# Optimization experiments

Hardware: AMD Instinct MI355X
Metric: run time of the kernel (lower is better)

## Reference

```python
import jax, jax.numpy as jnp
import numpy as np

C = 1024
H = 16
D = C // H  # head_dim = 64
FF = 4 * C


def setup_inputs() -> dict:
    key = jax.random.key(0)
    ks = jax.random.split(key, 10)
    s = lambda fan_in: 1.0 / np.sqrt(fan_in)
    return {
        "x": jax.random.normal(ks[0], (2, 2048, C), dtype=jnp.float32),
        "ln1_g": jnp.ones((C,), jnp.float32),
        "ln1_b": jnp.zeros((C,), jnp.float32),
        "w_qkv": jax.random.normal(ks[1], (C, 3 * C), jnp.float32) * s(C),
        "w_proj": jax.random.normal(ks[2], (C, C), jnp.float32) * s(C),
        "b_proj": jnp.zeros((C,), jnp.float32),
        "ln2_g": jnp.ones((C,), jnp.float32),
        "ln2_b": jnp.zeros((C,), jnp.float32),
        "w_fc1": jax.random.normal(ks[3], (C, FF), jnp.float32) * s(C),
        "b_fc1": jnp.zeros((FF,), jnp.float32),
        "w_fc2": jax.random.normal(ks[4], (FF, C), jnp.float32) * s(FF),
        "b_fc2": jnp.zeros((C,), jnp.float32),
    }


def _layernorm(x, g, b, eps=1e-5):
    mu = jnp.mean(x, axis=-1, keepdims=True)
    var = jnp.var(x, axis=-1, keepdims=True)
    return (x - mu) * jax.lax.rsqrt(var + eps) * g + b


def reference(x, ln1_g, ln1_b, w_qkv, w_proj, b_proj, ln2_g, ln2_b, w_fc1, b_fc1, w_fc2, b_fc2):
    B, N, _ = x.shape
    scale = D ** -0.5
    # --- attention sub-block (pre-LN) ---
    h = _layernorm(x, ln1_g, ln1_b)
    qkv = (h @ w_qkv).reshape(B, N, 3, H, D)
    q, k, v = jnp.moveaxis(qkv, 2, 0)          # each [B, N, H, D]
    attn = jnp.einsum("bnhd,bmhd->bhnm", q, k) * scale  # [B,H,N,N]
    attn = jax.nn.softmax(attn, axis=-1)
    o = jnp.einsum("bhnm,bmhd->bnhd", attn, v).reshape(B, N, C)
    x = x + o @ w_proj + b_proj
    # --- MLP sub-block (pre-LN) ---
    h = _layernorm(x, ln2_g, ln2_b)
    h = jax.nn.gelu(h @ w_fc1 + b_fc1, approximate=False)
    x = x + h @ w_fc2 + b_fc2
    return x
```

## Files before the change

kernel.cpp:

```cpp
#include <hip/hip_runtime.h>
#include <hip/hip_bf16.h>

typedef unsigned short u16;
typedef unsigned int u32;
typedef __attribute__((ext_vector_type(8))) short bf16x8;
typedef __attribute__((ext_vector_type(4))) float f32x4;
typedef __attribute__((ext_vector_type(4))) int   i32x4;
typedef __attribute__((ext_vector_type(4))) float fvec4;
typedef __attribute__((ext_vector_type(4))) unsigned int u32x4;

__device__ inline u16 f2bf(float f) {
    union { float f; unsigned u; } v; v.f = f;
    unsigned r = v.u + 0x7fffu + ((v.u >> 16) & 1u);
    return (u16)(r >> 16);
}

__device__ inline u32 cvtpk(float lo, float hi) {
    u32 r;
    asm("v_cvt_pk_bf16_f32 %0, %1, %2" : "=v"(r) : "v"(lo), "v"(hi));
    return r;
}

__device__ inline f32x4 mfma16(bf16x8 a, bf16x8 b, f32x4 c) {
    return __builtin_amdgcn_mfma_f32_16x16x32_bf16(a, b, c, 0, 0, 0);
}

__device__ inline void gload16(const void* g, void* l) {
    __builtin_amdgcn_global_load_lds(
        (const __attribute__((address_space(1))) unsigned int*)g,
        (__attribute__((address_space(3))) unsigned int*)l, 16, 0, 0);
}

__global__ __launch_bounds__(256)
void transpose_all(const float* __restrict__ w0, u16* __restrict__ o0,
                   const float* __restrict__ w1, u16* __restrict__ o1,
                   const float* __restrict__ w2, u16* __restrict__ o2,
                   const float* __restrict__ w3, u16* __restrict__ o3) {
    __shared__ float tile[32][33];
    int b = blockIdx.x;
    const float* in; u16* out; int K, N, local;
    if (b < 3072)      { in = w0; out = o0; K = 1024; N = 3072; local = b; }
    else if (b < 4096) { in = w1; out = o1; K = 1024; N = 1024; local = b - 3072; }
    else if (b < 8192) { in = w2; out = o2; K = 1024; N = 4096; local = b - 4096; }
    else               { in = w3; out = o3; K = 4096; N = 1024; local = b - 8192; }
    const int nx = N >> 5;
    const int n0 = (local % nx) * 32, k0 = (local / nx) * 32;
    const int x = threadIdx.x & 31, y = threadIdx.x >> 5;
    for (int i = 0; i < 4; ++i)
        tile[y + i * 8][x] = in[(size_t)(k0 + y + i * 8) * N + n0 + x];
    __syncthreads();
    for (int i = 0; i < 4; ++i) {
        int r = y + i * 8;
        out[(size_t)(n0 + r) * K + k0 + x] = f2bf(tile[x][r]);
    }
}

__global__ __launch_bounds__(256)
void vtrans(const u16* __restrict__ qkv, u16* __restrict__ vT) {
    __shared__ u32 tl[64][33];
    const int t0 = blockIdx.x * 64, f0 = blockIdx.y * 64;
    const int a = threadIdx.x & 31, yy = threadIdx.x >> 5;
    for (int i = 0; i < 8; ++i) {
        int t = yy + i * 8;
        tl[t][a] = *(const u32*)(qkv + (size_t)(t0 + t) * 3072 + 2048 + f0 + a * 2);
    }
    __syncthreads();
    for (int i = 0; i < 8; ++i) {
        int f = yy + i * 8;
        u32 lo = tl[2 * a][f >> 1], hi = tl[2 * a + 1][f >> 1];
        u32 r = (f & 1) ? ((lo >> 16) | (hi & 0xffff0000u))
                        : ((lo & 0xffffu) | (hi << 16));
        *(u32*)(vT + (size_t)(f0 + f) * 4096 + t0 + 2 * a) = r;
    }
}

__global__ __launch_bounds__(256)
void ln_kernel(const float* __restrict__ x, const float* __restrict__ g,
               const float* __restrict__ bvec, u16* __restrict__ out) {
    __shared__ float red[2][4];
    const int row = blockIdx.x, tid = threadIdx.x;
    const float* xr = x + (size_t)row * 1024;
    fvec4 v = *(const fvec4*)(xr + tid * 4);
    float s  = v[0] + v[1] + v[2] + v[3];
    float s2 = v[0]*v[0] + v[1]*v[1] + v[2]*v[2] + v[3]*v[3];
    for (int off = 1; off < 64; off <<= 1) {
        s  += __shfl_xor(s,  off);
        s2 += __shfl_xor(s2, off);
    }
    const int w = tid >> 6;
    if ((tid & 63) == 0) { red[0][w] = s; red[1][w] = s2; }
    __syncthreads();
    s  = red[0][0] + red[0][1] + red[0][2] + red[0][3];
    s2 = red[1][0] + red[1][1] + red[1][2] + red[1][3];
    const float mu  = s * (1.0f / 1024.0f);
    const float var = s2 * (1.0f / 1024.0f) - mu * mu;
    const float rstd = rsqrtf(var + 1e-5f);
    fvec4 gv = *(const fvec4*)(g + tid * 4);
    fvec4 bv = *(const fvec4*)(bvec + tid * 4);
    u16 o4[4];
    for (int i = 0; i < 4; ++i)
        o4[i] = f2bf((v[i] - mu) * rstd * gv[i] + bv[i]);
    u32 lo = (u32)o4[0] | ((u32)o4[1] << 16);
    u32 hi = (u32)o4[2] | ((u32)o4[3] << 16);
    u32* dst = (u32*)(out + (size_t)row * 1024 + tid * 4);
    dst[0] = lo; dst[1] = hi;
}

__global__ __launch_bounds__(256)
void reduce4(const float* __restrict__ p1, const float* __restrict__ p2,
             const float* __restrict__ p3, const float* __restrict__ bias,
             const float* __restrict__ res, float* __restrict__ out) {
    const size_t base = (size_t)blockIdx.x * 1024 + threadIdx.x * 4;
    fvec4 a = *(const fvec4*)(out + base);
    fvec4 b = *(const fvec4*)(p1 + base);
    fvec4 c = *(const fvec4*)(p2 + base);
    fvec4 d = *(const fvec4*)(p3 + base);
    fvec4 r = *(const fvec4*)(res + base);
    fvec4 bi = *(const fvec4*)(bias + threadIdx.x * 4);
    fvec4 o;
#pragma unroll
    for (int i = 0; i < 4; ++i) o[i] = ((a[i] + b[i]) + (c[i] + d[i])) + bi[i] + r[i];
    *(fvec4*)(out + base) = o;
}

template <int MODE, int WM, int WN, int MT, int NT, int NYP>
__global__ __launch_bounds__(256)
void gemm64(const u16* __restrict__ A, const u16* __restrict__ Bt,
            const float* __restrict__ bias, const float* __restrict__ res,
            void* __restrict__ out, int M, int N, int K) {
    constexpr int TM = WM * MT * 16;
    constexpr int TN = WN * NT * 16;
    constexpr int AJ = TM / 64;
    constexpr int BJ = TN / 64;
    static_assert(TM == 128, "swizzle assumes 32 M-tiles");
    __shared__ __attribute__((aligned(16))) u16 sA[2 * TM * 32];
    __shared__ __attribute__((aligned(16))) u16 sB[2 * TN * 32];
    const int id = blockIdx.x;
    const int j  = id >> 3;
    const int by = (id & 7) * NYP + (j >> 5);
    const int bx = j & 31;
    const int tid = threadIdx.x;
    const int lane = tid & 63, w = tid >> 6;
    const int wm = w / WN, wn = w % WN;
    const int q = lane >> 4, l16 = lane & 15;

    f32x4 acc[MT][NT];
#pragma unroll
    for (int i = 0; i < MT; ++i)
#pragma unroll
        for (int jj = 0; jj < NT; ++jj) acc[i][jj] = (f32x4)0.0f;

    const int sr = lane >> 2;
    const int kc = (lane & 3) * 8;
    const u16* gA[AJ];
    const u16* gB[BJ];
#pragma unroll
    for (int jj = 0; jj < AJ; ++jj)
        gA[jj] = A + (size_t)(bx * TM + (jj * 4 + w) * 16 + sr) * K + kc;
#pragma unroll
    for (int jj = 0; jj < BJ; ++jj)
        gB[jj] = Bt + (size_t)(by * TN + (jj * 4 + w) * 16 + sr) * K + kc;

    for (int k0 = 0; k0 < K; k0 += 64) {
#pragma unroll
        for (int kt = 0; kt < 2; ++kt) {
#pragma unroll
            for (int jj = 0; jj < AJ; ++jj)
                gload16(gA[jj] + k0 + kt * 32, &sA[kt * TM * 32 + (jj * 4 + w) * 512]);
#pragma unroll
            for (int jj = 0; jj < BJ; ++jj)
                gload16(gB[jj] + k0 + kt * 32, &sB[kt * TN * 32 + (jj * 4 + w) * 512]);
        }
        __syncthreads();
#pragma unroll
        for (int kt = 0; kt < 2; ++kt) {
            bf16x8 af[MT], bf[NT];
#pragma unroll
            for (int mt = 0; mt < MT; ++mt)
                af[mt] = *(const bf16x8*)&sA[kt * TM * 32 +
                         (wm * MT * 16 + mt * 16 + l16) * 32 + q * 8];
#pragma unroll
            for (int nt = 0; nt < NT; ++nt)
                bf[nt] = *(const bf16x8*)&sB[kt * TN * 32 +
                         (wn * NT * 16 + nt * 16 + l16) * 32 + q * 8];
#pragma unroll
            for (int mt = 0; mt < MT; ++mt)
#pragma unroll
                for (int nt = 0; nt < NT; ++nt)
                    acc[mt][nt] = mfma16(af[mt], bf[nt], acc[mt][nt]);
        }
        __syncthreads();
    }

#pragma unroll
    for (int mt = 0; mt < MT; ++mt)
#pragma unroll
        for (int nt = 0; nt < NT; ++nt)
#pragma unroll
            for (int r = 0; r < 4; ++r) {
                const int row = bx * TM + wm * MT * 16 + mt * 16 + q * 4 + r;
                const int col = by * TN + wn * NT * 16 + nt * 16 + l16;
                const size_t idx = (size_t)row * N + col;
                float v = acc[mt][nt][r];
                if (MODE == 0) {
                    ((u16*)out)[idx] = f2bf(v);
                } else if (MODE == 1) {
                    ((float*)out)[idx] = v + bias[col] + res[idx];
                } else {
                    float t = v + bias[col];
                    ((u16*)out)[idx] = f2bf(t * 0.5f * (1.0f + erff(t * 0.70710678118f)));
                }
            }
}

template <int MODE, int SPLIT>
__global__ __launch_bounds__(512)
void gemm256(const u16* __restrict__ A, const u16* __restrict__ Bt,
             const float* __restrict__ bias, const float* __restrict__ res,
             void* __restrict__ out,
             float* __restrict__ q1, float* __restrict__ q2, float* __restrict__ q3,
             int M, int N, int K, int Kc) {
    __shared__ __attribute__((aligned(16))) u16 sA[2][16384];
    __shared__ __attribute__((aligned(16))) u16 sB[2][16384];
    const int tid  = threadIdx.x;
    const int w    = tid >> 6, lane = tid & 63;
    const int wm   = w >> 2,  wn   = w & 3;
    const int q    = lane >> 4, l16 = lane & 15;
    const int w8   = w << 3,  l8   = lane >> 3;
    const int kch  = (lane & 7) ^ l8;

    const int nwg  = gridDim.x;
    const int id   = blockIdx.x;
    const int wgid = (id & 7) * (nwg >> 3) + (id >> 3);
    int bx, by, sp;
    if (SPLIT == 1) { bx = wgid & 15; by = wgid >> 4; sp = 0; }
    else            { bx = wgid & 15; by = (wgid >> 4) & 3; sp = wgid >> 6; }

    const u16* pAs = A  + (size_t)(bx * 256 + w8 + l8) * K + kch * 8 + (size_t)sp * Kc;
    const u16* pBs = Bt + (size_t)(by * 256 + w8 + l8) * K + kch * 8 + (size_t)sp * Kc;

    const int cs0  = ((q ^ (l16 & 7)) << 4);
    const int cs1  = cs0 ^ 64;
    const int aoff = (wm * 128 + l16) * 128;
    const int boff = (wn * 64  + l16) * 128;

    f32x4 acc[8][4];
#pragma unroll
    for (int m = 0; m < 8; ++m)
#pragma unroll
        for (int n = 0; n < 4; ++n) acc[m][n] = (f32x4)0.0f;

#define GISS(P, r0, k0, SH, b_) \
    gload16((P) + (size_t)((r0) * K + (k0)), &SH[b_][((r0) + w8) * 64])

    GISS(pBs, 0, 0, sB, 0);  GISS(pBs, 64, 0, sB, 0);
    GISS(pBs, 128, 0, sB, 0); GISS(pBs, 192, 0, sB, 0);
    GISS(pAs, 0, 0, sA, 0);  GISS(pAs, 64, 0, sA, 0);
    GISS(pAs, 128, 0, sA, 0); GISS(pAs, 192, 0, sA, 0);
    GISS(pBs, 0, 64, sB, 1); GISS(pBs, 64, 64, sB, 1);
    GISS(pBs, 128, 64, sB, 1); GISS(pBs, 192, 64, sB, 1);
    asm volatile("s_waitcnt vmcnt(4)" ::: "memory");
    __builtin_amdgcn_s_barrier();

    bf16x8 bfr[4][2];

#define PHASE(mq_, cb_, SP, SH, sb_, sr0, sk0) do {                          \
    const char* bA_ = (const char*)&sA[cb_][0] + aoff;                       \
    const char* bB_ = (const char*)&sB[cb_][0] + boff;                       \
    if ((mq_) == 0) {                                                        \
        _Pragma("unroll") for (int n = 0; n < 4; ++n) {                      \
            bfr[n][0] = *(const bf16x8*)(bB_ + n * 2048 + cs0);              \
            bfr[n][1] = *(const bf16x8*)(bB_ + n * 2048 + cs1);              \
        }                                                                    \
    }                                                                        \
    bf16x8 af_[2][2];                                                        \
    _Pragma("unroll") for (int mi = 0; mi < 2; ++mi) {                       \
        af_[mi][0] = *(const bf16x8*)(bA_ + (2 * (mq_) + mi) * 2048 + cs0);  \
        af_[mi][1] = *(const bf16x8*)(bA_ + (2 * (mq_) + mi) * 2048 + cs1);  \
    }                                                                        \
    GISS(SP, (sr0), (sk0), SH, sb_);                                         \
    GISS(SP, (sr0) + 64, (sk0), SH, sb_);                                    \
    __builtin_amdgcn_sched_barrier(0);   \
    __builtin_amdgcn_s_barrier();                                            \
    asm volatile("s_waitcnt lgkmcnt(0)" ::: "memory");                       \
    __builtin_amdgcn_sched_barrier(0);          \
    __builtin_amdgcn_s_setprio(1);                                           \
    _Pragma("unroll") for (int kt = 0; kt < 2; ++kt)                         \
        _Pragma("unroll") for (int mi = 0; mi < 2; ++mi)                     \
            _Pragma("unroll") for (int n = 0; n < 4; ++n)                    \
                acc[2 * (mq_) + mi][n] =                                     \
                    mfma16(af_[mi][kt], bfr[n][kt], acc[2 * (mq_) + mi][n]); \
    __builtin_amdgcn_s_setprio(0);                                           \
    if ((mq_) == 3) asm volatile("s_waitcnt vmcnt(4)" ::: "memory");         \
    __builtin_amdgcn_s_barrier();                                            \
} while (0)

    const int NI = Kc >> 7;
    for (int i = 0; i < NI; ++i) {
        const int kb  = i << 7;
        const int kA1 = kb + 64;
        const int kN  = (kb + 128 < Kc) ? kb + 128 : Kc - 64;
        const int kB1 = (kb + 192 < Kc) ? kb + 192 : Kc - 64;
        PHASE(0, 0, pAs, sA, 1, 0,   kA1);
        PHASE(1, 0, pAs, sA, 1, 128, kA1);
        PHASE(2, 0, pBs, sB, 0, 0,   kN);
        PHASE(3, 0, pBs, sB, 0, 128, kN);
        PHASE(0, 1, pAs, sA, 0, 0,   kN);
        PHASE(1, 1, pAs, sA, 0, 128, kN);
        PHASE(2, 1, pBs, sB, 1, 0,   kB1);
        PHASE(3, 1, pBs, sB, 1, 128, kB1);
    }
#undef PHASE
#undef GISS

    float* po = nullptr;
    if (MODE == 3)
        po = sp == 0 ? (float*)out : sp == 1 ? q1 : sp == 2 ? q2 : q3;

#pragma unroll
    for (int m = 0; m < 8; ++m)
#pragma unroll
        for (int n = 0; n < 4; ++n)
#pragma unroll
            for (int r = 0; r < 4; ++r) {
                const int row = bx * 256 + wm * 128 + m * 16 + q * 4 + r;
                const int col = by * 256 + wn * 64 + n * 16 + l16;
                const size_t idx = (size_t)row * N + col;
                float v = acc[m][n][r];
                if (MODE == 0) {
                    ((u16*)out)[idx] = f2bf(v);
                } else if (MODE == 1) {
                    ((float*)out)[idx] = v + bias[col] + res[idx];
                } else if (MODE == 2) {
                    float t = v + bias[col];
                    ((u16*)out)[idx] = f2bf(t * 0.5f * (1.0f + erff(t * 0.70710678118f)));
                } else {
                    po[idx] = v;
                }
            }
}

__global__ __launch_bounds__(256)
void attention3(const u16* __restrict__ qkv, const u16* __restrict__ vT,
                u16* __restrict__ o) {
    __shared__ __attribute__((aligned(16))) u16 sK[64][72];
    __shared__ __attribute__((aligned(16))) u16 sV[64][72];

    const int tid = threadIdx.x;
    const int lane = tid & 63, w = tid >> 6;
    const int qc = lane >> 4, l16 = lane & 15;
    const int bx = blockIdx.x;
    const int qt = bx & 15, h = (bx >> 4) & 15, b = bx >> 8;
    const int rowbase = qt * 128 + w * 32;

    bf16x8 aQ[2][2];
#pragma unroll
    for (int mtq = 0; mtq < 2; ++mtq)
#pragma unroll
        for (int kd = 0; kd < 2; ++kd)
            aQ[mtq][kd] = *(const bf16x8*)(qkv +
                (size_t)(b * 2048 + rowbase + mtq * 16 + l16) * 3072 +
                h * 64 + kd * 32 + qc * 8);

    f32x4 accO[2][4];
#pragma unroll
    for (int mtq = 0; mtq < 2; ++mtq)
#pragma unroll
        for (int dt = 0; dt < 4; ++dt) accO[mtq][dt] = (f32x4)0.0f;
    f32x4 accS[2];
    accS[0] = (f32x4)0.0f; accS[1] = (f32x4)0.0f;

    bf16x8 vone;
#pragma unroll
    for (int i = 0; i < 8; ++i) vone[i] = (short)0x3F80;

    const int srr = tid >> 3;
    const int sc8 = (tid & 7) * 8;
    const u16* gK = qkv + (size_t)(b * 2048 + srr) * 3072 + 1024 + h * 64 + sc8;
    const u16* gV = vT + (size_t)(h * 64 + srr) * 4096 + b * 2048 + sc8;

    i32x4 cK[2], cV[2];
    cK[0] = *(const i32x4*)gK;
    cK[1] = *(const i32x4*)(gK + (size_t)32 * 3072);
    cV[0] = *(const i32x4*)gV;
    cV[1] = *(const i32x4*)(gV + (size_t)32 * 4096);

    const int sig_base = ((l16 >> 2) << 3) + (l16 & 3);

    for (int kc = 0; kc < 32; ++kc) {
        __syncthreads();
        *(i32x4*)&sK[srr][sc8]      = cK[0];
        *(i32x4*)&sK[srr + 32][sc8] = cK[1];
        *(i32x4*)&sV[srr][sc8]      = cV[0];
        *(i32x4*)&sV[srr + 32][sc8] = cV[1];
        const int kn = (kc + 1 < 32) ? kc + 1 : 31;
        i32x4 nK[2], nV[2];
        nK[0] = *(const i32x4*)(gK + (size_t)kn * 64 * 3072);
        nK[1] = *(const i32x4*)(gK + ((size_t)kn * 64 + 32) * 3072);
        nV[0] = *(const i32x4*)(gV + kn * 64);
        nV[1] = *(const i32x4*)(gV + (size_t)32 * 4096 + kn * 64);
        __syncthreads();

        bf16x8 kf[4][2];
#pragma unroll
        for (int mk = 0; mk < 4; ++mk) {
            const int krow = ((mk & 1) << 5) + ((mk >> 1) << 2) + sig_base;
            kf[mk][0] = *(const bf16x8*)&sK[krow][qc * 8];
            kf[mk][1] = *(const bf16x8*)&sK[krow][32 + qc * 8];
        }

        f32x4 s[2][4];
#pragma unroll
        for (int mtq = 0; mtq < 2; ++mtq)
#pragma unroll
            for (int mk = 0; mk < 4; ++mk) {
                f32x4 z = (f32x4)0.0f;
                z = mfma16(kf[mk][0], aQ[mtq][0], z);
                z = mfma16(kf[mk][1], aQ[mtq][1], z);
                s[mtq][mk] = z;
            }

        bf16x8 pf[2][2];
#pragma unroll
        for (int mtq = 0; mtq < 2; ++mtq) {
#pragma unroll
            for (int mk = 0; mk < 4; ++mk)
#pragma unroll
                for (int r = 0; r < 4; ++r)
                    s[mtq][mk][r] = __expf(s[mtq][mk][r] * 0.125f);
#pragma unroll
            for (int kt = 0; kt < 2; ++kt) {
                u32x4 pw;
                pw[0] = cvtpk(s[mtq][kt][0],     s[mtq][kt][1]);
                pw[1] = cvtpk(s[mtq][kt][2],     s[mtq][kt][3]);
                pw[2] = cvtpk(s[mtq][2 + kt][0], s[mtq][2 + kt][1]);
                pw[3] = cvtpk(s[mtq][2 + kt][2], s[mtq][2 + kt][3]);
                pf[mtq][kt] = *(const bf16x8*)&pw;
            }
        }

#pragma unroll
        for (int kt = 0; kt < 2; ++kt) {
#pragma unroll
            for (int dt = 0; dt < 4; ++dt) {
                bf16x8 vf = *(const bf16x8*)&sV[dt * 16 + l16][kt * 32 + qc * 8];
#pragma unroll
                for (int mtq = 0; mtq < 2; ++mtq)
                    accO[mtq][dt] = mfma16(pf[mtq][kt], vf, accO[mtq][dt]);
            }
#pragma unroll
            for (int mtq = 0; mtq < 2; ++mtq)
                accS[mtq] = mfma16(pf[mtq][kt], vone, accS[mtq]);
        }

        cK[0] = nK[0]; cK[1] = nK[1];
        cV[0] = nV[0]; cV[1] = nV[1];
    }

#pragma unroll
    for (int mtq = 0; mtq < 2; ++mtq)
#pragma unroll
        for (int r = 0; r < 4; ++r) {
            const float inv = 1.0f / accS[mtq][r];
            const size_t tok = (size_t)b * 2048 + rowbase + mtq * 16 + qc * 4 + r;
#pragma unroll
            for (int dt = 0; dt < 4; ++dt)
                o[tok * 1024 + h * 64 + dt * 16 + l16] = f2bf(accO[mtq][dt][r] * inv);
        }
}

extern "C" void kernel_launch(void* const* d_in, const int* in_sizes, int n_in,
                              void* d_out, int out_size, void* d_ws, size_t ws_size,
                              hipStream_t stream) {
    const float* x      = (const float*)d_in[0];
    const float* ln1_g  = (const float*)d_in[1];
    const float* ln1_b  = (const float*)d_in[2];
    const float* w_qkv  = (const float*)d_in[3];
    const float* w_proj = (const float*)d_in[4];
    const float* b_proj = (const float*)d_in[5];
    const float* ln2_g  = (const float*)d_in[6];
    const float* ln2_b  = (const float*)d_in[7];
    const float* w_fc1  = (const float*)d_in[8];
    const float* b_fc1  = (const float*)d_in[9];
    const float* w_fc2  = (const float*)d_in[10];
    const float* b_fc2  = (const float*)d_in[11];
    float* out = (float*)d_out;

    char* ws = (char*)d_ws;
    u16*   wqkvT  = (u16*)(ws + 0);
    u16*   wprojT = (u16*)(ws + 6291456);
    u16*   wfc1T  = (u16*)(ws + 8388608);
    u16*   wfc2T  = (u16*)(ws + 16777216);
    u16*   hA     = (u16*)(ws + 25165824);
    u16*   qkv    = (u16*)(ws + 33554432);
    float* x1     = (float*)(ws + 58720256);
    u16*   gbuf   = (u16*)(ws + 75497472);
    u16*   vT     = (u16*)(ws + 75497472);
    float* p1     = (float*)(ws + 0);
    float* p2     = (float*)(ws + 25165824);
    float* p3     = (float*)(ws + 41943040);

    dim3 blk(256);
    transpose_all<<<12288, blk, 0, stream>>>(w_qkv, wqkvT, w_proj, wprojT,
                                             w_fc1, wfc1T, w_fc2, wfc2T);

    ln_kernel<<<4096, blk, 0, stream>>>(x, ln1_g, ln1_b, hA);
    gemm256<0, 1><<<192, dim3(512), 0, stream>>>(hA, wqkvT, nullptr, nullptr, qkv,
                                                 nullptr, nullptr, nullptr, 4096, 3072, 1024, 1024);
    vtrans<<<dim3(64, 16), blk, 0, stream>>>(qkv, vT);
    attention3<<<512, blk, 0, stream>>>(qkv, vT, hA);
    gemm64<1, 4, 1, 2, 4, 2><<<512, blk, 0, stream>>>(hA, wprojT, b_proj, x, x1, 4096, 1024, 1024);

    u16* h2 = qkv;
    ln_kernel<<<4096, blk, 0, stream>>>(x1, ln2_g, ln2_b, h2);
    gemm256<2, 1><<<256, dim3(512), 0, stream>>>(h2, wfc1T, b_fc1, nullptr, gbuf,
                                                 nullptr, nullptr, nullptr, 4096, 4096, 1024, 1024);
    gemm256<3, 4><<<256, dim3(512), 0, stream>>>(gbuf, wfc2T, nullptr, nullptr, out,
                                                 p1, p2, p3, 4096, 1024, 4096, 1024);
    reduce4<<<4096, blk, 0, stream>>>(p1, p2, p3, b_fc2, x1, out);
}
```

Measured before the change: 357.0 us.

## Restructure GEMM main loop into two half-tile phases per K step

```diff
diff --git a/kernel.cpp b/kernel.cpp
--- a/kernel.cpp
+++ b/kernel.cpp
@@ -253,64 +253,72 @@
 #define GISS(P, r0, k0, SH, b_) \
     gload16((P) + (size_t)((r0) * K + (k0)), &SH[b_][((r0) + w8) * 64])
 
-    GISS(pBs, 0, 0, sB, 0);  GISS(pBs, 64, 0, sB, 0);
+    GISS(pBs, 0, 0, sB, 0);   GISS(pBs, 64, 0, sB, 0);
     GISS(pBs, 128, 0, sB, 0); GISS(pBs, 192, 0, sB, 0);
-    GISS(pAs, 0, 0, sA, 0);  GISS(pAs, 64, 0, sA, 0);
+    GISS(pAs, 0, 0, sA, 0);   GISS(pAs, 64, 0, sA, 0);
     GISS(pAs, 128, 0, sA, 0); GISS(pAs, 192, 0, sA, 0);
-    GISS(pBs, 0, 64, sB, 1); GISS(pBs, 64, 64, sB, 1);
-    GISS(pBs, 128, 64, sB, 1); GISS(pBs, 192, 64, sB, 1);
+    GISS(pBs, 0, 64, sB, 1);  GISS(pBs, 64, 64, sB, 1);
+    GISS(pBs, 128, 64, sB, 1);GISS(pBs, 192, 64, sB, 1);
     asm volatile("s_waitcnt vmcnt(4)" ::: "memory");
     __builtin_amdgcn_s_barrier();
 
-    bf16x8 bfr[4][2];
-
-#define PHASE(mq_, cb_, SP, SH, sb_, sr0, sk0) do {                          \
-    const char* bA_ = (const char*)&sA[cb_][0] + aoff;                       \
-    const char* bB_ = (const char*)&sB[cb_][0] + boff;                       \
-    if ((mq_) == 0) {                                                        \
-        _Pragma("unroll") for (int n = 0; n < 4; ++n) {                      \
-            bfr[n][0] = *(const bf16x8*)(bB_ + n * 2048 + cs0);              \
-            bfr[n][1] = *(const bf16x8*)(bB_ + n * 2048 + cs1);              \
-        }                                                                    \
-    }                                                                        \
-    bf16x8 af_[2][2];                                                        \
-    _Pragma("unroll") for (int mi = 0; mi < 2; ++mi) {                       \
-        af_[mi][0] = *(const bf16x8*)(bA_ + (2 * (mq_) + mi) * 2048 + cs0);  \
-        af_[mi][1] = *(const bf16x8*)(bA_ + (2 * (mq_) + mi) * 2048 + cs1);  \
-    }                                                                        \
-    GISS(SP, (sr0), (sk0), SH, sb_);                                         \
-    GISS(SP, (sr0) + 64, (sk0), SH, sb_);                                    \
-    __builtin_amdgcn_sched_barrier(0);   \
-    __builtin_amdgcn_s_barrier();                                            \
-    asm volatile("s_waitcnt lgkmcnt(0)" ::: "memory");                       \
-    __builtin_amdgcn_sched_barrier(0);          \
-    __builtin_amdgcn_s_setprio(1);                                           \
-    _Pragma("unroll") for (int kt = 0; kt < 2; ++kt)                         \
-        _Pragma("unroll") for (int mi = 0; mi < 2; ++mi)                     \
-            _Pragma("unroll") for (int n = 0; n < 4; ++n)                    \
-                acc[2 * (mq_) + mi][n] =                                     \
-                    mfma16(af_[mi][kt], bfr[n][kt], acc[2 * (mq_) + mi][n]); \
-    __builtin_amdgcn_s_setprio(0);                                           \
-    if ((mq_) == 3) asm volatile("s_waitcnt vmcnt(4)" ::: "memory");         \
-    __builtin_amdgcn_s_barrier();                                            \
-} while (0)
-
-    const int NI = Kc >> 7;
-    for (int i = 0; i < NI; ++i) {
-        const int kb  = i << 7;
-        const int kA1 = kb + 64;
-        const int kN  = (kb + 128 < Kc) ? kb + 128 : Kc - 64;
-        const int kB1 = (kb + 192 < Kc) ? kb + 192 : Kc - 64;
-        PHASE(0, 0, pAs, sA, 1, 0,   kA1);
-        PHASE(1, 0, pAs, sA, 1, 128, kA1);
-        PHASE(2, 0, pBs, sB, 0, 0,   kN);
-        PHASE(3, 0, pBs, sB, 0, 128, kN);
-        PHASE(0, 1, pAs, sA, 0, 0,   kN);
-        PHASE(1, 1, pAs, sA, 0, 128, kN);
-        PHASE(2, 1, pBs, sB, 1, 0,   kB1);
-        PHASE(3, 1, pBs, sB, 1, 128, kB1);
-    }
-#undef PHASE
+    const int NT_ = Kc >> 6;
+    for (int t = 0; t < NT_; ++t) {
+        const int b  = t & 1;
+        const char* bA_ = (const char*)&sA[b][0] + aoff;
+        const char* bB_ = (const char*)&sB[b][0] + boff;
+        const int kA = (t + 1 < NT_ ? t + 1 : t) << 6;
+        const int kB = (t + 2 < NT_ ? t + 2 : t) << 6;
+
+        bf16x8 bfr[4][2];
+#pragma unroll
+        for (int n = 0; n < 4; ++n) {
+            bfr[n][0] = *(const bf16x8*)(bB_ + n * 2048 + cs0);
+            bfr[n][1] = *(const bf16x8*)(bB_ + n * 2048 + cs1);
+        }
+        bf16x8 af[4][2];
+#pragma unroll
+        for (int m = 0; m < 4; ++m) {
+            af[m][0] = *(const bf16x8*)(bA_ + m * 2048 + cs0);
+            af[m][1] = *(const bf16x8*)(bA_ + m * 2048 + cs1);
+        }
+        if (b) { GISS(pAs, 0, kA, sA, 0); GISS(pAs, 64, kA, sA, 0);
+                 GISS(pAs, 128, kA, sA, 0); GISS(pAs, 192, kA, sA, 0); }
+        else   { GISS(pAs, 0, kA, sA, 1); GISS(pAs, 64, kA, sA, 1);
+                 GISS(pAs, 128, kA, sA, 1); GISS(pAs, 192, kA, sA, 1); }
+        __builtin_amdgcn_s_setprio(1);
+#pragma unroll
+        for (int kt = 0; kt < 2; ++kt)
+#pragma unroll
+            for (int m = 0; m < 4; ++m)
+#pragma unroll
+                for (int n = 0; n < 4; ++n)
+                    acc[m][n] = mfma16(af[m][kt], bfr[n][kt], acc[m][n]);
+        __builtin_amdgcn_s_setprio(0);
+        __builtin_amdgcn_s_barrier();
+
+        bf16x8 ag[4][2];
+#pragma unroll
+        for (int m = 0; m < 4; ++m) {
+            ag[m][0] = *(const bf16x8*)(bA_ + (4 + m) * 2048 + cs0);
+            ag[m][1] = *(const bf16x8*)(bA_ + (4 + m) * 2048 + cs1);
+        }
+        if (b) { GISS(pBs, 0, kB, sB, 1); GISS(pBs, 64, kB, sB, 1);
+                 GISS(pBs, 128, kB, sB, 1); GISS(pBs, 192, kB, sB, 1); }
+        else   { GISS(pBs, 0, kB, sB, 0); GISS(pBs, 64, kB, sB, 0);
+                 GISS(pBs, 128, kB, sB, 0); GISS(pBs, 192, kB, sB, 0); }
+        __builtin_amdgcn_s_setprio(1);
+#pragma unroll
+        for (int kt = 0; kt < 2; ++kt)
+#pragma unroll
+            for (int m = 0; m < 4; ++m)
+#pragma unroll
+                for (int n = 0; n < 4; ++n)
+                    acc[4 + m][n] = mfma16(ag[m][kt], bfr[n][kt], acc[4 + m][n]);
+        __builtin_amdgcn_s_setprio(0);
+        asm volatile("s_waitcnt vmcnt(4)" ::: "memory");
+        __builtin_amdgcn_s_barrier();
+    }
 #undef GISS
 
     float* po = nullptr;
```

Measured after the change: 348.0 us. 2.5% less time.
